# Kernel tuning notes

Measured on AMD Instinct MI355X. Metric: run time of the kernel, lower is better.

The kernel has to match this reference:

```python
import jax, jax.numpy as jnp
import numpy as np

HEAD_NUM = 16

def setup_inputs() -> dict:
    key = jax.random.key(0)
    ks = jax.random.split(key, 5)
    B, N, D = 2, 2048, 1024
    x = jax.random.normal(ks[0], (B, N, D), dtype=jnp.float32)
    scale = 0.02
    W_q = jax.random.normal(ks[1], (D, D), dtype=jnp.float32) * scale
    W_k = jax.random.normal(ks[2], (D, D), dtype=jnp.float32) * scale
    W_v = jax.random.normal(ks[3], (D, D), dtype=jnp.float32) * scale
    W_o = jax.random.normal(ks[4], (D, D), dtype=jnp.float32) * scale
    return {"x": x, "W_q": W_q, "W_k": W_k, "W_v": W_v, "W_o": W_o}

def reference(x, W_q, W_k, W_v, W_o):
    B, N, D = x.shape
    H = HEAD_NUM
    hd = D // H  # head_dim
    inv_sqrt_hd = 1.0 / np.sqrt(hd).astype(np.float32)

    def split_head(t):
        # einops 'b n (d h) -> b h n d' : head index is the INNER factor
        return t.reshape(B, N, hd, H).transpose(0, 3, 1, 2)  # [B,H,N,hd]

    # nn.Linear(bias=False): y = x @ W.T
    Q = split_head(x @ W_q.T)
    K = split_head(x @ W_k.T)
    V = split_head(x @ W_v.T)

    scores = jnp.einsum('bhnd,bhmd->bhnm', Q, K) * inv_sqrt_hd  # [B,H,N,N]
    attn = jax.nn.softmax(scores, axis=-1)
    heads = jnp.einsum('bhnm,bhmd->bhnd', attn, V)  # [B,H,N,hd]

    # einops 'b h n d -> b n (h d)' : head index is the OUTER factor here
    concat = heads.transpose(0, 2, 1, 3).reshape(B, N, D)
    return concat @ W_o.T
```

## Files before the change

kernel.cpp:

```cpp
#include <hip/hip_runtime.h>
#include <hip/hip_bf16.h>

typedef __bf16 bf16_t;
typedef __attribute__((ext_vector_type(8))) __bf16 bf16x8;
typedef __attribute__((ext_vector_type(4))) __bf16 bf16x4;
typedef __attribute__((ext_vector_type(4))) float f32x4;
typedef __attribute__((ext_vector_type(16))) float f32x16;

#define MFMA16(A,B,C) __builtin_amdgcn_mfma_f32_16x16x32_bf16((A),(B),(C),0,0,0)
#define MFMA32(A,B,C) __builtin_amdgcn_mfma_f32_32x32x16_bf16((A),(B),(C),0,0,0)

#define BATCH 2
#define SEQ 2048
#define DMODEL 1024
#define NHEAD 16
#define HDIM 64
#define MROWS (BATCH * SEQ)

__device__ __forceinline__ void async16(const bf16_t* g, bf16_t* l) {
    __builtin_amdgcn_global_load_lds(
        (const __attribute__((address_space(1))) unsigned int*)g,
        (__attribute__((address_space(3))) unsigned int*)l, 16, 0, 0);
}

__device__ __forceinline__ bf16x8 ldsA32(const bf16_t* base, int row, int chunk) {
    return *(const bf16x8*)&base[row * 32 + ((chunk ^ ((row >> 1) & 3)) << 3)];
}

__device__ __forceinline__ unsigned pk(float a, float b) {
    union { unsigned u; bf16_t h[2]; } t;
    t.h[0] = (bf16_t)a;
    t.h[1] = (bf16_t)b;
    return t.u;
}

__device__ __forceinline__ void plane32_swap(unsigned& d, unsigned& s) {
    asm("v_permlane32_swap_b32 %0, %1" : "+v"(d), "+v"(s));
}

__global__ void split_kernel(const float* __restrict__ x, const float* __restrict__ Wq,
                             const float* __restrict__ Wk, const float* __restrict__ Wv,
                             const float* __restrict__ Wo, bf16_t* __restrict__ xh,
                             bf16_t* __restrict__ wh) {
    int blk = blockIdx.x;
    if (blk < 4096) {
        int i = blk * 256 + threadIdx.x;
        f32x4 v = ((const f32x4*)x)[i];
        bf16x4 h;
#pragma unroll
        for (int c = 0; c < 4; ++c) h[c] = (bf16_t)v[c];
        ((bf16x4*)xh)[i] = h;
        return;
    }
    int e = blk - 4096;
    int z = e >> 10;
    int i = (e & 1023) * 256 + threadIdx.x;
    const float* src = (z == 0) ? Wq : (z == 1) ? Wk : (z == 2) ? Wv : Wo;
    const float scale = (z == 0) ? 0.125f * 1.44269504088896f : 1.0f;
    int row = i >> 8, col4 = i & 255;
    int r_src;
    if (z < 3) {
        int h = row >> 6, d = row & 63;
        r_src = 16 * d + h;
    } else {
        r_src = row;
    }
    f32x4 v = ((const f32x4*)src)[r_src * 256 + col4];
    bf16x4 h4;
#pragma unroll
    for (int c = 0; c < 4; ++c) h4[c] = (bf16_t)(v[c] * scale);
    ((bf16x4*)(wh + (size_t)z * DMODEL * DMODEL))[i] = h4;
}

__global__ __launch_bounds__(256)
void gemm_qkv_kernel(const bf16_t* __restrict__ Ah, const bf16_t* __restrict__ Bh0,
                     bf16_t* __restrict__ Coh0, bf16_t* __restrict__ Vt,
                     int M, int Nn, int Kk) {
    __shared__ __align__(16) bf16_t smem[2][8192];

    const int id = blockIdx.x;
    const int xcd = id & 7;
    const int t = id >> 3;
    const int n0i = t & 7;
    const int u = t >> 3;
    const int z = u >> 2;
    const int m0g = u & 3;
    const int m0 = (m0g * 8 + xcd) * 128;
    const int n0 = n0i * 128;

    const bf16_t* Bh = Bh0 + (size_t)z * Nn * Kk;
    const int tid = threadIdx.x;
    const int wave = tid >> 6, lane = tid & 63, lq = lane >> 4, ln = lane & 15;
    const int wr = wave >> 1, wc = wave & 1;

    const bf16_t* g_ptr[4];
    int l_off[4];
#pragma unroll
    for (int q = 0; q < 4; ++q) {
        int e = wave * 4 + q;
        int a = e >> 3, uu = e & 7;
        int C = uu * 64 + lane;
        int r = C >> 2, p = C & 3;
        int c = p ^ ((r >> 1) & 3);
        g_ptr[q] = (a == 0 ? Ah + (size_t)(m0 + r) * Kk
                           : Bh + (size_t)(n0 + r) * Kk) + c * 8;
        l_off[q] = a * 4096 + uu * 512;
    }

    f32x4 acc[4][4] = {};

#pragma unroll
    for (int q = 0; q < 4; ++q)
        async16(g_ptr[q], &smem[0][l_off[q]]);

    const int NIT = Kk / 32;
    for (int j = 0; j < NIT; ++j) {
        __syncthreads();
        if (j + 1 < NIT) {
#pragma unroll
            for (int q = 0; q < 4; ++q)
                async16(g_ptr[q] + (j + 1) * 32, &smem[(j + 1) & 1][l_off[q]]);
        }
        const bf16_t* cur = smem[j & 1];

        bf16x8 ah[4], bh[4];
#pragma unroll
        for (int tt = 0; tt < 4; ++tt) {
            ah[tt] = ldsA32(cur, wr * 64 + tt * 16 + ln, lq);
            bh[tt] = ldsA32(cur + 4096, wc * 64 + tt * 16 + ln, lq);
        }
#pragma unroll
        for (int tm = 0; tm < 4; ++tm)
#pragma unroll
            for (int tn = 0; tn < 4; ++tn)
                acc[tm][tn] = MFMA16(ah[tm], bh[tn], acc[tm][tn]);
    }

    if (z != 2) {
#pragma unroll
        for (int tm = 0; tm < 4; ++tm)
#pragma unroll
            for (int tn = 0; tn < 4; ++tn)
#pragma unroll
                for (int p = 0; p < 4; ++p) {
                    int gm = m0 + wr * 64 + tm * 16 + lq * 4 + p;
                    int gn = n0 + wc * 64 + tn * 16 + ln;
                    Coh0[(size_t)z * M * Nn + (size_t)gm * Nn + gn] =
                        (bf16_t)acc[tm][tn][p];
                }
    } else {
#pragma unroll
        for (int tm = 0; tm < 4; ++tm)
#pragma unroll
            for (int tn = 0; tn < 4; ++tn) {
                int gn = n0 + wc * 64 + tn * 16 + ln;
                int hh = gn >> 6, dd = gn & 63;
                int gm0 = m0 + wr * 64 + tm * 16 + lq * 4;
                int bb = gm0 >> 11, nn = gm0 & 2047;
                bf16x4 v4;
#pragma unroll
                for (int p = 0; p < 4; ++p) v4[p] = (bf16_t)acc[tm][tn][p];
                *(bf16x4*)&Vt[(((size_t)(bb * NHEAD + hh)) * HDIM + dd) * SEQ + nn] = v4;
            }
    }
}

__global__ __launch_bounds__(256)
void gemm_out_kernel(const bf16_t* __restrict__ Ah, const bf16_t* __restrict__ Bh,
                     float* __restrict__ Cf, int M, int Nn, int Kk) {
    __shared__ __align__(16) bf16_t smem[2][6144];

    const int id = blockIdx.x;
    const int xcd = id & 7;
    const int t = id >> 3;
    const int n0i = t & 7;
    const int m0g = t >> 3;
    const int m0 = (m0g * 8 + xcd) * 64;
    const int n0 = n0i * 128;

    const int tid = threadIdx.x;
    const int wave = tid >> 6, lane = tid & 63, lq = lane >> 4, ln = lane & 15;
    const int wr = wave >> 1, wc = wave & 1;

    const bf16_t* g_ptr[3];
    int l_off[3];
#pragma unroll
    for (int q = 0; q < 3; ++q) {
        int e = wave * 3 + q;
        const bf16_t* arr;
        int u, rowbase, lb;
        if (e < 4) { arr = Ah; u = e;     rowbase = m0; lb = 0; }
        else       { arr = Bh; u = e - 4; rowbase = n0; lb = 2048; }
        int r = u * 16 + (lane >> 2), p = lane & 3;
        int c = p ^ ((r >> 1) & 3);
        g_ptr[q] = arr + (size_t)(rowbase + r) * Kk + c * 8;
        l_off[q] = lb + u * 512;
    }

    f32x4 acc[2][4] = {};

#pragma unroll
    for (int q = 0; q < 3; ++q)
        async16(g_ptr[q], &smem[0][l_off[q]]);

    const int NIT = Kk / 32;
    for (int j = 0; j < NIT; ++j) {
        __syncthreads();
        if (j + 1 < NIT) {
#pragma unroll
            for (int q = 0; q < 3; ++q)
                async16(g_ptr[q] + (j + 1) * 32, &smem[(j + 1) & 1][l_off[q]]);
        }
        const bf16_t* cur = smem[j & 1];

        bf16x8 ah[2], bh[4];
#pragma unroll
        for (int tt = 0; tt < 2; ++tt)
            ah[tt] = ldsA32(cur, wr * 32 + tt * 16 + ln, lq);
#pragma unroll
        for (int tt = 0; tt < 4; ++tt)
            bh[tt] = ldsA32(cur + 2048, wc * 64 + tt * 16 + ln, lq);
#pragma unroll
        for (int tm = 0; tm < 2; ++tm)
#pragma unroll
            for (int tn = 0; tn < 4; ++tn)
                acc[tm][tn] = MFMA16(ah[tm], bh[tn], acc[tm][tn]);
    }

#pragma unroll
    for (int tm = 0; tm < 2; ++tm)
#pragma unroll
        for (int tn = 0; tn < 4; ++tn)
#pragma unroll
            for (int p = 0; p < 4; ++p) {
                int gm = m0 + wr * 32 + tm * 16 + lq * 4 + p;
                int gn = n0 + wc * 64 + tn * 16 + ln;
                Cf[(size_t)gm * Nn + gn] = acc[tm][tn][p];
            }
}

__global__ __launch_bounds__(512, 4)
void attn_kernel(const bf16_t* __restrict__ Qh, const bf16_t* __restrict__ Kh,
                 const bf16_t* __restrict__ Vt, bf16_t* __restrict__ Ch) {
    __shared__ __align__(16) bf16_t smem[2][2][8192];

    const int id = blockIdx.x;
    const int bh = ((id >> 7) << 3) | (id & 7);
    const int qt = (id >> 3) & 15;
    const int b = bh >> 4, h = bh & 15;
    const int q0 = qt * 128;
    const int tid = threadIdx.x;
    const int g = tid >> 8;
    const int wv = (tid >> 6) & 3;
    const int lane = tid & 63;
    const int ln32 = lane & 31, hl = lane >> 5;

    bf16x8 qfh[4];
    {
        size_t qrow = ((size_t)(b * SEQ + q0 + wv * 32 + ln32)) * DMODEL +
                      h * HDIM + hl * 8;
#pragma unroll
        for (int c = 0; c < 4; ++c)
            qfh[c] = *(const bf16x8*)&Qh[qrow + c * 16];
    }

    const int xrow = ln32 * 64;
    int xc[4];
#pragma unroll
    for (int c = 0; c < 4; ++c)
        xc[c] = (((2 * c + hl) ^ (ln32 & 7)) << 3) + xrow;

    bf16_t* gsm = &smem[g][0][0];
    const bf16_t* g_cur[4];
    int l_off[4];
    size_t g_step[4];
#pragma unroll
    for (int q = 0; q < 4; ++q) {
        int e = wv * 4 + q;
        int a = e >> 3, u = e & 7;
        int r = u * 8 + (lane >> 3), p = lane & 7;
        int c = p ^ (r & 7);
        if (a == 0) {
            g_cur[q] = Kh + ((size_t)(b * SEQ + g * 1024 + r)) * DMODEL +
                       h * HDIM + c * 8;
            l_off[q] = u * 512;
            g_step[q] = (size_t)64 * DMODEL;
        } else {
            g_cur[q] = Vt + ((size_t)(bh * HDIM + r)) * SEQ + g * 1024 + c * 8;
            l_off[q] = 4096 + u * 512;
            g_step[q] = 64;
        }
    }

    f32x16 o[2];
#pragma unroll
    for (int dt = 0; dt < 2; ++dt)
#pragma unroll
        for (int r = 0; r < 16; ++r) o[dt][r] = 0.0f;
    float rs0 = 0.0f, rs1 = 0.0f, rs2 = 0.0f, rs3 = 0.0f;

#pragma unroll
    for (int q = 0; q < 4; ++q) {
        async16(g_cur[q], gsm + l_off[q]);
        g_cur[q] += g_step[q];
    }

    for (int j = 0; j < 16; ++j) {
        __syncthreads();
        if (j < 15) {
#pragma unroll
            for (int q = 0; q < 4; ++q) {
                async16(g_cur[q], gsm + ((j + 1) & 1) * 8192 + l_off[q]);
                g_cur[q] += g_step[q];
            }
        }
        const bf16_t* Kc = gsm + (j & 1) * 8192;
        const bf16_t* Vc = Kc + 4096;

        bf16x8 pfrag[4];
#pragma unroll
        for (int kt = 0; kt < 2; ++kt) {
            f32x16 st;
#pragma unroll
            for (int r = 0; r < 16; ++r) st[r] = 0.0f;
            __builtin_amdgcn_s_setprio(1);
#pragma unroll
            for (int c = 0; c < 4; ++c) {
                bf16x8 kh = *(const bf16x8*)&Kc[kt * 2048 + xc[c]];
                st = MFMA32(kh, qfh[c], st);
            }
            __builtin_amdgcn_s_setprio(0);
            float pexp[16];
#pragma unroll
            for (int r = 0; r < 16; ++r) {
                pexp[r] = __builtin_amdgcn_exp2f(st[r]);
            }
            rs0 += pexp[0] + pexp[4] + pexp[8] + pexp[12];
            rs1 += pexp[1] + pexp[5] + pexp[9] + pexp[13];
            rs2 += pexp[2] + pexp[6] + pexp[10] + pexp[14];
            rs3 += pexp[3] + pexp[7] + pexp[11] + pexp[15];
#pragma unroll
            for (int s1 = 0; s1 < 2; ++s1) {
                unsigned lo01 = pk(pexp[8 * s1 + 0], pexp[8 * s1 + 1]);
                unsigned lo23 = pk(pexp[8 * s1 + 2], pexp[8 * s1 + 3]);
                unsigned hi01 = pk(pexp[8 * s1 + 4], pexp[8 * s1 + 5]);
                unsigned hi23 = pk(pexp[8 * s1 + 6], pexp[8 * s1 + 7]);
                plane32_swap(lo01, hi01);
                plane32_swap(lo23, hi23);
                union { bf16x8 v; unsigned u[4]; } outv;
                outv.u[0] = lo01;
                outv.u[1] = lo23;
                outv.u[2] = hi01;
                outv.u[3] = hi23;
                pfrag[kt * 2 + s1] = outv.v;
            }
        }
        __builtin_amdgcn_s_setprio(1);
#pragma unroll
        for (int s = 0; s < 4; ++s) {
            bf16x8 va0 = *(const bf16x8*)&Vc[xc[s]];
            bf16x8 va1 = *(const bf16x8*)&Vc[2048 + xc[s]];
            o[0] = MFMA32(va0, pfrag[s], o[0]);
            o[1] = MFMA32(va1, pfrag[s], o[1]);
        }
        __builtin_amdgcn_s_setprio(0);
    }

    float rs = (rs0 + rs1) + (rs2 + rs3);
    rs += __shfl_xor(rs, 32);

    __syncthreads();
    float* cbuf = (float*)smem;
    float* rbuf = cbuf + 8192;
    if (g == 1) {
#pragma unroll
        for (int dt = 0; dt < 2; ++dt)
#pragma unroll
            for (int r = 0; r < 16; ++r) {
                int d = dt * 32 + (r & 3) + 8 * (r >> 2) + 4 * hl;
                cbuf[d * 128 + wv * 32 + ln32] = o[dt][r];
            }
        if (hl == 0) rbuf[wv * 32 + ln32] = rs;
    }
    __syncthreads();
    float inv = 0.0f;
    if (g == 0) {
#pragma unroll
        for (int dt = 0; dt < 2; ++dt)
#pragma unroll
            for (int r = 0; r < 16; ++r) {
                int d = dt * 32 + (r & 3) + 8 * (r >> 2) + 4 * hl;
                o[dt][r] += cbuf[d * 128 + wv * 32 + ln32];
            }
        inv = 1.0f / (rs + rbuf[wv * 32 + ln32]);
    }
    __syncthreads();
    float* fbuf = (float*)smem;
    if (g == 0) {
#pragma unroll
        for (int dh = 0; dh < 2; ++dh)
#pragma unroll
            for (int r = 0; r < 16; ++r) {
                int d_loc = (r & 3) + 8 * (r >> 2) + 4 * hl;
                fbuf[dh * 4224 + wv * 1056 + ln32 * 33 + d_loc] = o[dh][r] * inv;
            }
    }
    __syncthreads();
    {
        int gw = tid >> 6;
        int dh = gw >> 2, w = gw & 3;
#pragma unroll
        for (int qq = 0; qq < 16; ++qq) {
            int qrow = hl * 16 + qq;
            float v = fbuf[dh * 4224 + w * 1056 + qrow * 33 + ln32];
            size_t gidx = ((size_t)(b * SEQ + q0 + w * 32 + qrow)) * DMODEL +
                          h * HDIM + dh * 32 + ln32;
            Ch[gidx] = (bf16_t)v;
        }
    }
}

extern "C" void kernel_launch(void* const* d_in, const int* in_sizes, int n_in,
                              void* d_out, int out_size, void* d_ws, size_t ws_size,
                              hipStream_t stream) {
    const float* x  = (const float*)d_in[0];
    const float* Wq = (const float*)d_in[1];
    const float* Wk = (const float*)d_in[2];
    const float* Wv = (const float*)d_in[3];
    const float* Wo = (const float*)d_in[4];
    float* out = (float*)d_out;

    char* ws = (char*)d_ws;
    size_t off = 0;
    auto alloc = [&](size_t bytes) -> bf16_t* {
        bf16_t* p = (bf16_t*)(ws + off);
        off += (bytes + 255) & ~(size_t)255;
        return p;
    };
    const size_t XE = (size_t)MROWS * DMODEL;
    const size_t WE = (size_t)DMODEL * DMODEL;

    bf16_t* xh  = alloc(XE * 2);
    bf16_t* wh  = alloc(4 * WE * 2);
    bf16_t* qnh = alloc(3 * XE * 2);
    bf16_t* vth = alloc(XE * 2);
    bf16_t* ch  = alloc(XE * 2);
    (void)ws_size; (void)in_sizes; (void)n_in; (void)out_size;

    split_kernel<<<8192, 256, 0, stream>>>(x, Wq, Wk, Wv, Wo, xh, wh);

    gemm_qkv_kernel<<<768, 256, 0, stream>>>(xh, wh, qnh, vth, MROWS, DMODEL, DMODEL);

    attn_kernel<<<512, 512, 0, stream>>>(qnh, qnh + XE, vth, ch);

    gemm_out_kernel<<<512, 256, 0, stream>>>(ch, wh + 3 * WE, out, MROWS, DMODEL, DMODEL);
}
```

Baseline: 174.1 us.

## Split attention KV range across four wave groups with 1024-thread blocks

The attention kernel now uses 1024 threads per block and splits the key/value sequence four ways instead of two. Each group processes 32-key tiles with a new swizzled V layout in smaller LDS buffers. Partial outputs and row sums are combined through a serial three-step shared-memory reduction. This adds intra-block parallelism and more waves to hide latency, at the cost of extra reduction barriers, a per-wave loop over the same 16 iterations with half the work each, and a launch_bounds of (1024,8) that may constrain registers.

```diff
diff --git a/kernel.cpp b/kernel.cpp
--- a/kernel.cpp
+++ b/kernel.cpp
@@ -239,10 +239,10 @@
             }
 }
 
-__global__ __launch_bounds__(512, 4)
+__global__ __launch_bounds__(1024, 8)
 void attn_kernel(const bf16_t* __restrict__ Qh, const bf16_t* __restrict__ Kh,
                  const bf16_t* __restrict__ Vt, bf16_t* __restrict__ Ch) {
-    __shared__ __align__(16) bf16_t smem[2][2][8192];
+    __shared__ __align__(16) bf16_t smem[4][2][4096];
 
     const int id = blockIdx.x;
     const int bh = ((id >> 7) << 3) | (id & 7);
@@ -264,31 +264,36 @@
             qfh[c] = *(const bf16x8*)&Qh[qrow + c * 16];
     }
 
-    const int xrow = ln32 * 64;
-    int xc[4];
+    int xcK[4];
 #pragma unroll
     for (int c = 0; c < 4; ++c)
-        xc[c] = (((2 * c + hl) ^ (ln32 & 7)) << 3) + xrow;
+        xcK[c] = (((2 * c + hl) ^ (ln32 & 7)) << 3) + ln32 * 64;
+    int xcV[2];
+#pragma unroll
+    for (int s = 0; s < 2; ++s)
+        xcV[s] = (((2 * s + hl) ^ ((ln32 >> 1) & 3)) << 3) + ln32 * 32;
 
     bf16_t* gsm = &smem[g][0][0];
-    const bf16_t* g_cur[4];
-    int l_off[4];
-    size_t g_step[4];
-#pragma unroll
-    for (int q = 0; q < 4; ++q) {
-        int e = wv * 4 + q;
-        int a = e >> 3, u = e & 7;
-        int r = u * 8 + (lane >> 3), p = lane & 7;
-        int c = p ^ (r & 7);
+    const bf16_t* g_cur[2];
+    int l_off[2];
+    size_t g_step[2];
+#pragma unroll
+    for (int q = 0; q < 2; ++q) {
+        int e = wv * 2 + q;
+        int a = e >> 2, u = e & 3;
         if (a == 0) {
-            g_cur[q] = Kh + ((size_t)(b * SEQ + g * 1024 + r)) * DMODEL +
+            int r = u * 8 + (lane >> 3), p = lane & 7;
+            int c = p ^ (r & 7);
+            g_cur[q] = Kh + ((size_t)(b * SEQ + g * 512 + r)) * DMODEL +
                        h * HDIM + c * 8;
             l_off[q] = u * 512;
-            g_step[q] = (size_t)64 * DMODEL;
+            g_step[q] = (size_t)32 * DMODEL;
         } else {
-            g_cur[q] = Vt + ((size_t)(bh * HDIM + r)) * SEQ + g * 1024 + c * 8;
-            l_off[q] = 4096 + u * 512;
-            g_step[q] = 64;
+            int r = u * 16 + (lane >> 2), p = lane & 3;
+            int c = p ^ ((r >> 1) & 3);
+            g_cur[q] = Vt + ((size_t)(bh * HDIM + r)) * SEQ + g * 512 + c * 8;
+            l_off[q] = 2048 + u * 512;
+            g_step[q] = 32;
         }
     }
 
@@ -300,7 +305,7 @@
     float rs0 = 0.0f, rs1 = 0.0f, rs2 = 0.0f, rs3 = 0.0f;
 
 #pragma unroll
-    for (int q = 0; q < 4; ++q) {
+    for (int q = 0; q < 2; ++q) {
         async16(g_cur[q], gsm + l_off[q]);
         g_cur[q] += g_step[q];
     }
@@ -309,57 +314,53 @@
         __syncthreads();
         if (j < 15) {
 #pragma unroll
-            for (int q = 0; q < 4; ++q) {
-                async16(g_cur[q], gsm + ((j + 1) & 1) * 8192 + l_off[q]);
+            for (int q = 0; q < 2; ++q) {
+                async16(g_cur[q], gsm + ((j + 1) & 1) * 4096 + l_off[q]);
                 g_cur[q] += g_step[q];
             }
         }
-        const bf16_t* Kc = gsm + (j & 1) * 8192;
-        const bf16_t* Vc = Kc + 4096;
-
-        bf16x8 pfrag[4];
-#pragma unroll
-        for (int kt = 0; kt < 2; ++kt) {
-            f32x16 st;
-#pragma unroll
-            for (int r = 0; r < 16; ++r) st[r] = 0.0f;
-            __builtin_amdgcn_s_setprio(1);
-#pragma unroll
-            for (int c = 0; c < 4; ++c) {
-                bf16x8 kh = *(const bf16x8*)&Kc[kt * 2048 + xc[c]];
-                st = MFMA32(kh, qfh[c], st);
-            }
-            __builtin_amdgcn_s_setprio(0);
-            float pexp[16];
-#pragma unroll
-            for (int r = 0; r < 16; ++r) {
-                pexp[r] = __builtin_amdgcn_exp2f(st[r]);
-            }
-            rs0 += pexp[0] + pexp[4] + pexp[8] + pexp[12];
-            rs1 += pexp[1] + pexp[5] + pexp[9] + pexp[13];
-            rs2 += pexp[2] + pexp[6] + pexp[10] + pexp[14];
-            rs3 += pexp[3] + pexp[7] + pexp[11] + pexp[15];
-#pragma unroll
-            for (int s1 = 0; s1 < 2; ++s1) {
-                unsigned lo01 = pk(pexp[8 * s1 + 0], pexp[8 * s1 + 1]);
-                unsigned lo23 = pk(pexp[8 * s1 + 2], pexp[8 * s1 + 3]);
-                unsigned hi01 = pk(pexp[8 * s1 + 4], pexp[8 * s1 + 5]);
-                unsigned hi23 = pk(pexp[8 * s1 + 6], pexp[8 * s1 + 7]);
-                plane32_swap(lo01, hi01);
-                plane32_swap(lo23, hi23);
-                union { bf16x8 v; unsigned u[4]; } outv;
-                outv.u[0] = lo01;
-                outv.u[1] = lo23;
-                outv.u[2] = hi01;
-                outv.u[3] = hi23;
-                pfrag[kt * 2 + s1] = outv.v;
-            }
-        }
+        const bf16_t* Kc = gsm + (j & 1) * 4096;
+        const bf16_t* Vc = Kc + 2048;
+
+        f32x16 st;
+#pragma unroll
+        for (int r = 0; r < 16; ++r) st[r] = 0.0f;
         __builtin_amdgcn_s_setprio(1);
 #pragma unroll
-        for (int s = 0; s < 4; ++s) {
-            bf16x8 va0 = *(const bf16x8*)&Vc[xc[s]];
-            bf16x8 va1 = *(const bf16x8*)&Vc[2048 + xc[s]];
+        for (int c = 0; c < 4; ++c) {
+            bf16x8 kh = *(const bf16x8*)&Kc[xcK[c]];
+            st = MFMA32(kh, qfh[c], st);
+        }
+        __builtin_amdgcn_s_setprio(0);
+        float pexp[16];
+#pragma unroll
+        for (int r = 0; r < 16; ++r)
+            pexp[r] = __builtin_amdgcn_exp2f(st[r]);
+        rs0 += pexp[0] + pexp[4] + pexp[8] + pexp[12];
+        rs1 += pexp[1] + pexp[5] + pexp[9] + pexp[13];
+        rs2 += pexp[2] + pexp[6] + pexp[10] + pexp[14];
+        rs3 += pexp[3] + pexp[7] + pexp[11] + pexp[15];
+        bf16x8 pfrag[2];
+#pragma unroll
+        for (int s1 = 0; s1 < 2; ++s1) {
+            unsigned lo01 = pk(pexp[8 * s1 + 0], pexp[8 * s1 + 1]);
+            unsigned lo23 = pk(pexp[8 * s1 + 2], pexp[8 * s1 + 3]);
+            unsigned hi01 = pk(pexp[8 * s1 + 4], pexp[8 * s1 + 5]);
+            unsigned hi23 = pk(pexp[8 * s1 + 6], pexp[8 * s1 + 7]);
+            plane32_swap(lo01, hi01);
+            plane32_swap(lo23, hi23);
+            union { bf16x8 v; unsigned u[4]; } outv;
+            outv.u[0] = lo01;
+            outv.u[1] = lo23;
+            outv.u[2] = hi01;
+            outv.u[3] = hi23;
+            pfrag[s1] = outv.v;
+        }
+        __builtin_amdgcn_s_setprio(1);
+#pragma unroll
+        for (int s = 0; s < 2; ++s) {
+            bf16x8 va0 = *(const bf16x8*)&Vc[xcV[s]];
+            bf16x8 va1 = *(const bf16x8*)&Vc[1024 + xcV[s]];
             o[0] = MFMA32(va0, pfrag[s], o[0]);
             o[1] = MFMA32(va1, pfrag[s], o[1]);
         }
@@ -372,29 +373,32 @@
     __syncthreads();
     float* cbuf = (float*)smem;
     float* rbuf = cbuf + 8192;
-    if (g == 1) {
-#pragma unroll
-        for (int dt = 0; dt < 2; ++dt)
-#pragma unroll
-            for (int r = 0; r < 16; ++r) {
-                int d = dt * 32 + (r & 3) + 8 * (r >> 2) + 4 * hl;
-                cbuf[d * 128 + wv * 32 + ln32] = o[dt][r];
-            }
-        if (hl == 0) rbuf[wv * 32 + ln32] = rs;
-    }
-    __syncthreads();
-    float inv = 0.0f;
-    if (g == 0) {
-#pragma unroll
-        for (int dt = 0; dt < 2; ++dt)
-#pragma unroll
-            for (int r = 0; r < 16; ++r) {
-                int d = dt * 32 + (r & 3) + 8 * (r >> 2) + 4 * hl;
-                o[dt][r] += cbuf[d * 128 + wv * 32 + ln32];
-            }
-        inv = 1.0f / (rs + rbuf[wv * 32 + ln32]);
-    }
-    __syncthreads();
+    for (int gg = 1; gg < 4; ++gg) {
+        if (g == gg) {
+#pragma unroll
+            for (int dt = 0; dt < 2; ++dt)
+#pragma unroll
+                for (int r = 0; r < 16; ++r) {
+                    int d = dt * 32 + (r & 3) + 8 * (r >> 2) + 4 * hl;
+                    cbuf[d * 128 + wv * 32 + ln32] = o[dt][r];
+                }
+            if (hl == 0) rbuf[wv * 32 + ln32] = rs;
+        }
+        __syncthreads();
+        if (g == 0) {
+#pragma unroll
+            for (int dt = 0; dt < 2; ++dt)
+#pragma unroll
+                for (int r = 0; r < 16; ++r) {
+                    int d = dt * 32 + (r & 3) + 8 * (r >> 2) + 4 * hl;
+                    o[dt][r] += cbuf[d * 128 + wv * 32 + ln32];
+                }
+            rs += rbuf[wv * 32 + ln32];
+        }
+        __syncthreads();
+    }
+    float inv = (g == 0) ? 1.0f / rs : 0.0f;
+
     float* fbuf = (float*)smem;
     if (g == 0) {
 #pragma unroll
@@ -408,10 +412,10 @@
     __syncthreads();
     {
         int gw = tid >> 6;
-        int dh = gw >> 2, w = gw & 3;
-#pragma unroll
-        for (int qq = 0; qq < 16; ++qq) {
-            int qrow = hl * 16 + qq;
+        int dh = gw >> 3, w = (gw >> 1) & 3, hq = gw & 1;
+#pragma unroll
+        for (int qq = 0; qq < 8; ++qq) {
+            int qrow = hl * 16 + hq * 8 + qq;
             float v = fbuf[dh * 4224 + w * 1056 + qrow * 33 + ln32];
             size_t gidx = ((size_t)(b * SEQ + q0 + w * 32 + qrow)) * DMODEL +
                           h * HDIM + dh * 32 + ln32;
@@ -451,7 +455,7 @@
 
     gemm_qkv_kernel<<<768, 256, 0, stream>>>(xh, wh, qnh, vth, MROWS, DMODEL, DMODEL);
 
-    attn_kernel<<<512, 512, 0, stream>>>(qnh, qnh + XE, vth, ch);
+    attn_kernel<<<512, 1024, 0, stream>>>(qnh, qnh + XE, vth, ch);
 
     gemm_out_kernel<<<512, 256, 0, stream>>>(ch, wh + 3 * WE, out, MROWS, DMODEL, DMODEL);
 }
```

After: 428.7 us. 146% more time.

## Process two query sub-tiles per wave in attention to reuse K/V fragments

Applied to the files above, without the earlier changes.

The attention kernel now runs 256 threads per block instead of 512. Each wave handles 64 query rows as two 32-row sub-tiles, so every K and V fragment read from LDS feeds twice as many MFMAs. Each wave issues 8 async loads per tile instead of 4, and the epilogue reduction and writeback are reindexed to match. This cuts LDS read traffic and instruction overhead per MFMA, but doubles the accumulator and Q-fragment registers per wave and halves the waves available to hide latency.

```diff
diff --git a/kernel.cpp b/kernel.cpp
--- a/kernel.cpp
+++ b/kernel.cpp
@@ -36,6 +36,32 @@
 
 __device__ __forceinline__ void plane32_swap(unsigned& d, unsigned& s) {
     asm("v_permlane32_swap_b32 %0, %1" : "+v"(d), "+v"(s));
+}
+
+__device__ __forceinline__ void sm_pack(const f32x16& st, float* rsp, bf16x8* pf) {
+    float pexp[16];
+#pragma unroll
+    for (int r = 0; r < 16; ++r)
+        pexp[r] = __builtin_amdgcn_exp2f(st[r]);
+    rsp[0] += pexp[0] + pexp[4] + pexp[8] + pexp[12];
+    rsp[1] += pexp[1] + pexp[5] + pexp[9] + pexp[13];
+    rsp[2] += pexp[2] + pexp[6] + pexp[10] + pexp[14];
+    rsp[3] += pexp[3] + pexp[7] + pexp[11] + pexp[15];
+#pragma unroll
+    for (int s1 = 0; s1 < 2; ++s1) {
+        unsigned lo01 = pk(pexp[8 * s1 + 0], pexp[8 * s1 + 1]);
+        unsigned lo23 = pk(pexp[8 * s1 + 2], pexp[8 * s1 + 3]);
+        unsigned hi01 = pk(pexp[8 * s1 + 4], pexp[8 * s1 + 5]);
+        unsigned hi23 = pk(pexp[8 * s1 + 6], pexp[8 * s1 + 7]);
+        plane32_swap(lo01, hi01);
+        plane32_swap(lo23, hi23);
+        union { bf16x8 v; unsigned u[4]; } outv;
+        outv.u[0] = lo01;
+        outv.u[1] = lo23;
+        outv.u[2] = hi01;
+        outv.u[3] = hi23;
+        pf[s1] = outv.v;
+    }
 }
 
 __global__ void split_kernel(const float* __restrict__ x, const float* __restrict__ Wq,
@@ -239,7 +265,7 @@
             }
 }
 
-__global__ __launch_bounds__(512, 4)
+__global__ __launch_bounds__(256, 2)
 void attn_kernel(const bf16_t* __restrict__ Qh, const bf16_t* __restrict__ Kh,
                  const bf16_t* __restrict__ Vt, bf16_t* __restrict__ Ch) {
     __shared__ __align__(16) bf16_t smem[2][2][8192];
@@ -250,18 +276,19 @@
     const int b = bh >> 4, h = bh & 15;
     const int q0 = qt * 128;
     const int tid = threadIdx.x;
-    const int g = tid >> 8;
-    const int wv = (tid >> 6) & 3;
+    const int g = tid >> 7;
+    const int wv = (tid >> 6) & 1;
     const int lane = tid & 63;
     const int ln32 = lane & 31, hl = lane >> 5;
 
-    bf16x8 qfh[4];
-    {
-        size_t qrow = ((size_t)(b * SEQ + q0 + wv * 32 + ln32)) * DMODEL +
+    bf16x8 qfh[2][4];
+#pragma unroll
+    for (int qs = 0; qs < 2; ++qs) {
+        size_t qrow = ((size_t)(b * SEQ + q0 + wv * 64 + qs * 32 + ln32)) * DMODEL +
                       h * HDIM + hl * 8;
 #pragma unroll
         for (int c = 0; c < 4; ++c)
-            qfh[c] = *(const bf16x8*)&Qh[qrow + c * 16];
+            qfh[qs][c] = *(const bf16x8*)&Qh[qrow + c * 16];
     }
 
     const int xrow = ln32 * 64;
@@ -271,151 +298,155 @@
         xc[c] = (((2 * c + hl) ^ (ln32 & 7)) << 3) + xrow;
 
     bf16_t* gsm = &smem[g][0][0];
-    const bf16_t* g_cur[4];
-    int l_off[4];
-    size_t g_step[4];
-#pragma unroll
-    for (int q = 0; q < 4; ++q) {
-        int e = wv * 4 + q;
-        int a = e >> 3, u = e & 7;
-        int r = u * 8 + (lane >> 3), p = lane & 7;
-        int c = p ^ (r & 7);
-        if (a == 0) {
-            g_cur[q] = Kh + ((size_t)(b * SEQ + g * 1024 + r)) * DMODEL +
-                       h * HDIM + c * 8;
-            l_off[q] = u * 512;
-            g_step[q] = (size_t)64 * DMODEL;
+    const bf16_t* gb;
+    size_t ustep, jstep;
+    int lb;
+    {
+        int r0 = lane >> 3, p = lane & 7;
+        int c = p ^ (r0 & 7);
+        if (wv == 0) {
+            gb = Kh + ((size_t)(b * SEQ + g * 1024 + r0)) * DMODEL +
+                 h * HDIM + c * 8;
+            ustep = (size_t)8 * DMODEL;
+            jstep = (size_t)64 * DMODEL;
+            lb = 0;
         } else {
-            g_cur[q] = Vt + ((size_t)(bh * HDIM + r)) * SEQ + g * 1024 + c * 8;
-            l_off[q] = 4096 + u * 512;
-            g_step[q] = 64;
-        }
-    }
-
-    f32x16 o[2];
-#pragma unroll
-    for (int dt = 0; dt < 2; ++dt)
-#pragma unroll
-        for (int r = 0; r < 16; ++r) o[dt][r] = 0.0f;
-    float rs0 = 0.0f, rs1 = 0.0f, rs2 = 0.0f, rs3 = 0.0f;
-
-#pragma unroll
-    for (int q = 0; q < 4; ++q) {
-        async16(g_cur[q], gsm + l_off[q]);
-        g_cur[q] += g_step[q];
-    }
+            gb = Vt + ((size_t)(bh * HDIM + r0)) * SEQ + g * 1024 + c * 8;
+            ustep = (size_t)8 * SEQ;
+            jstep = 64;
+            lb = 4096;
+        }
+    }
+
+    f32x16 o[2][2];
+#pragma unroll
+    for (int qs = 0; qs < 2; ++qs)
+#pragma unroll
+        for (int dt = 0; dt < 2; ++dt)
+#pragma unroll
+            for (int r = 0; r < 16; ++r) o[qs][dt][r] = 0.0f;
+    float rsA[4] = {0.f, 0.f, 0.f, 0.f};
+    float rsB[4] = {0.f, 0.f, 0.f, 0.f};
+
+#pragma unroll
+    for (int u = 0; u < 8; ++u)
+        async16(gb + u * ustep, gsm + lb + u * 512);
+    gb += jstep;
 
     for (int j = 0; j < 16; ++j) {
         __syncthreads();
         if (j < 15) {
 #pragma unroll
-            for (int q = 0; q < 4; ++q) {
-                async16(g_cur[q], gsm + ((j + 1) & 1) * 8192 + l_off[q]);
-                g_cur[q] += g_step[q];
-            }
+            for (int u = 0; u < 8; ++u)
+                async16(gb + u * ustep, gsm + ((j + 1) & 1) * 8192 + lb + u * 512);
+            gb += jstep;
         }
         const bf16_t* Kc = gsm + (j & 1) * 8192;
         const bf16_t* Vc = Kc + 4096;
 
-        bf16x8 pfrag[4];
+        bf16x8 pfA[4], pfB[4];
 #pragma unroll
         for (int kt = 0; kt < 2; ++kt) {
-            f32x16 st;
-#pragma unroll
-            for (int r = 0; r < 16; ++r) st[r] = 0.0f;
+            bf16x8 kh[4];
+#pragma unroll
+            for (int c = 0; c < 4; ++c)
+                kh[c] = *(const bf16x8*)&Kc[kt * 2048 + xc[c]];
+            f32x16 s0, s1;
+#pragma unroll
+            for (int r = 0; r < 16; ++r) { s0[r] = 0.0f; s1[r] = 0.0f; }
             __builtin_amdgcn_s_setprio(1);
 #pragma unroll
-            for (int c = 0; c < 4; ++c) {
-                bf16x8 kh = *(const bf16x8*)&Kc[kt * 2048 + xc[c]];
-                st = MFMA32(kh, qfh[c], st);
-            }
+            for (int c = 0; c < 4; ++c)
+                s0 = MFMA32(kh[c], qfh[0][c], s0);
+#pragma unroll
+            for (int c = 0; c < 4; ++c)
+                s1 = MFMA32(kh[c], qfh[1][c], s1);
             __builtin_amdgcn_s_setprio(0);
-            float pexp[16];
-#pragma unroll
-            for (int r = 0; r < 16; ++r) {
-                pexp[r] = __builtin_amdgcn_exp2f(st[r]);
-            }
-            rs0 += pexp[0] + pexp[4] + pexp[8] + pexp[12];
-            rs1 += pexp[1] + pexp[5] + pexp[9] + pexp[13];
-            rs2 += pexp[2] + pexp[6] + pexp[10] + pexp[14];
-            rs3 += pexp[3] + pexp[7] + pexp[11] + pexp[15];
-#pragma unroll
-            for (int s1 = 0; s1 < 2; ++s1) {
-                unsigned lo01 = pk(pexp[8 * s1 + 0], pexp[8 * s1 + 1]);
-                unsigned lo23 = pk(pexp[8 * s1 + 2], pexp[8 * s1 + 3]);
-                unsigned hi01 = pk(pexp[8 * s1 + 4], pexp[8 * s1 + 5]);
-                unsigned hi23 = pk(pexp[8 * s1 + 6], pexp[8 * s1 + 7]);
-                plane32_swap(lo01, hi01);
-                plane32_swap(lo23, hi23);
-                union { bf16x8 v; unsigned u[4]; } outv;
-                outv.u[0] = lo01;
-                outv.u[1] = lo23;
-                outv.u[2] = hi01;
-                outv.u[3] = hi23;
-                pfrag[kt * 2 + s1] = outv.v;
-            }
+            sm_pack(s0, rsA, &pfA[kt * 2]);
+            sm_pack(s1, rsB, &pfB[kt * 2]);
         }
         __builtin_amdgcn_s_setprio(1);
 #pragma unroll
         for (int s = 0; s < 4; ++s) {
             bf16x8 va0 = *(const bf16x8*)&Vc[xc[s]];
             bf16x8 va1 = *(const bf16x8*)&Vc[2048 + xc[s]];
-            o[0] = MFMA32(va0, pfrag[s], o[0]);
-            o[1] = MFMA32(va1, pfrag[s], o[1]);
+            o[0][0] = MFMA32(va0, pfA[s], o[0][0]);
+            o[0][1] = MFMA32(va1, pfA[s], o[0][1]);
+            o[1][0] = MFMA32(va0, pfB[s], o[1][0]);
+            o[1][1] = MFMA32(va1, pfB[s], o[1][1]);
         }
         __builtin_amdgcn_s_setprio(0);
     }
 
-    float rs = (rs0 + rs1) + (rs2 + rs3);
-    rs += __shfl_xor(rs, 32);
+    float rs[2];
+    rs[0] = (rsA[0] + rsA[1]) + (rsA[2] + rsA[3]);
+    rs[1] = (rsB[0] + rsB[1]) + (rsB[2] + rsB[3]);
+#pragma unroll
+    for (int qs = 0; qs < 2; ++qs)
+        rs[qs] += __shfl_xor(rs[qs], 32);
 
     __syncthreads();
     float* cbuf = (float*)smem;
     float* rbuf = cbuf + 8192;
     if (g == 1) {
 #pragma unroll
-        for (int dt = 0; dt < 2; ++dt)
-#pragma unroll
-            for (int r = 0; r < 16; ++r) {
-                int d = dt * 32 + (r & 3) + 8 * (r >> 2) + 4 * hl;
-                cbuf[d * 128 + wv * 32 + ln32] = o[dt][r];
-            }
-        if (hl == 0) rbuf[wv * 32 + ln32] = rs;
+        for (int qs = 0; qs < 2; ++qs)
+#pragma unroll
+            for (int dt = 0; dt < 2; ++dt)
+#pragma unroll
+                for (int r = 0; r < 16; ++r) {
+                    int d = dt * 32 + (r & 3) + 8 * (r >> 2) + 4 * hl;
+                    cbuf[d * 128 + wv * 64 + qs * 32 + ln32] = o[qs][dt][r];
+                }
+        if (hl == 0) {
+            rbuf[wv * 64 + ln32] = rs[0];
+            rbuf[wv * 64 + 32 + ln32] = rs[1];
+        }
     }
     __syncthreads();
-    float inv = 0.0f;
+    float inv[2] = {0.0f, 0.0f};
     if (g == 0) {
 #pragma unroll
-        for (int dt = 0; dt < 2; ++dt)
-#pragma unroll
-            for (int r = 0; r < 16; ++r) {
-                int d = dt * 32 + (r & 3) + 8 * (r >> 2) + 4 * hl;
-                o[dt][r] += cbuf[d * 128 + wv * 32 + ln32];
-            }
-        inv = 1.0f / (rs + rbuf[wv * 32 + ln32]);
+        for (int qs = 0; qs < 2; ++qs) {
+#pragma unroll
+            for (int dt = 0; dt < 2; ++dt)
+#pragma unroll
+                for (int r = 0; r < 16; ++r) {
+                    int d = dt * 32 + (r & 3) + 8 * (r >> 2) + 4 * hl;
+                    o[qs][dt][r] += cbuf[d * 128 + wv * 64 + qs * 32 + ln32];
+                }
+            inv[qs] = 1.0f / (rs[qs] + rbuf[wv * 64 + qs * 32 + ln32]);
+        }
     }
     __syncthreads();
     float* fbuf = (float*)smem;
     if (g == 0) {
 #pragma unroll
-        for (int dh = 0; dh < 2; ++dh)
-#pragma unroll
-            for (int r = 0; r < 16; ++r) {
-                int d_loc = (r & 3) + 8 * (r >> 2) + 4 * hl;
-                fbuf[dh * 4224 + wv * 1056 + ln32 * 33 + d_loc] = o[dh][r] * inv;
-            }
+        for (int qs = 0; qs < 2; ++qs)
+#pragma unroll
+            for (int dh = 0; dh < 2; ++dh)
+#pragma unroll
+                for (int r = 0; r < 16; ++r) {
+                    int d_loc = (r & 3) + 8 * (r >> 2) + 4 * hl;
+                    fbuf[dh * 4224 + (wv * 2 + qs) * 1056 + ln32 * 33 + d_loc] =
+                        o[qs][dh][r] * inv[qs];
+                }
     }
     __syncthreads();
     {
         int gw = tid >> 6;
-        int dh = gw >> 2, w = gw & 3;
-#pragma unroll
-        for (int qq = 0; qq < 16; ++qq) {
-            int qrow = hl * 16 + qq;
-            float v = fbuf[dh * 4224 + w * 1056 + qrow * 33 + ln32];
-            size_t gidx = ((size_t)(b * SEQ + q0 + w * 32 + qrow)) * DMODEL +
-                          h * HDIM + dh * 32 + ln32;
-            Ch[gidx] = (bf16_t)v;
+        int dh = gw >> 1, wpair = gw & 1;
+#pragma unroll
+        for (int ww = 0; ww < 2; ++ww) {
+            int w = wpair * 2 + ww;
+#pragma unroll
+            for (int qq = 0; qq < 16; ++qq) {
+                int qrow = hl * 16 + qq;
+                float v = fbuf[dh * 4224 + w * 1056 + qrow * 33 + ln32];
+                size_t gidx = ((size_t)(b * SEQ + q0 + w * 32 + qrow)) * DMODEL +
+                              h * HDIM + dh * 32 + ln32;
+                Ch[gidx] = (bf16_t)v;
+            }
         }
     }
 }
@@ -451,7 +482,7 @@
 
     gemm_qkv_kernel<<<768, 256, 0, stream>>>(xh, wh, qnh, vth, MROWS, DMODEL, DMODEL);
 
-    attn_kernel<<<512, 512, 0, stream>>>(qnh, qnh + XE, vth, ch);
+    attn_kernel<<<512, 256, 0, stream>>>(qnh, qnh + XE, vth, ch);
 
     gemm_out_kernel<<<512, 256, 0, stream>>>(ch, wh + 3 * WE, out, MROWS, DMODEL, DMODEL);
 }
```

After: 175.0 us. About the same (+0.5%).
